# Kernel optimization log

Hardware: AMD Instinct MI355X
Metric: run time of the kernel (lower is better)

The kernel has to match this reference:

```python
import jax, jax.numpy as jnp
import numpy as np

B, H, W_SP, C = 256, 14, 14, 768
NUM_CLASSES = 701


def setup_inputs() -> dict:
    key = jax.random.key(0)
    k1, k2, k3 = jax.random.split(key, 3)
    x1 = jax.random.normal(k1, (B, H, W_SP, C), dtype=jnp.float32)
    x2 = jax.random.normal(k2, (B, H, W_SP, C), dtype=jnp.float32)
    W = jax.random.normal(k3, (C, NUM_CLASSES), dtype=jnp.float32) * 0.02
    b = jnp.zeros((NUM_CLASSES,), dtype=jnp.float32)
    return {"x1": x1, "x2": x2, "W": W, "b": b}


def _sgm(feats):
    """Vectorized SGM: per-sample sort by normalized token energy, gap-based
    split index, masked means for background/foreground. feats: [B, N, C]."""
    n = feats.shape[1]
    M = feats.sum(axis=-1)                                  # [B, N] token energies
    mn = M.min(axis=-1, keepdims=True)
    mx = M.max(axis=-1, keepdims=True)
    Mn = (M - mn) / (mx - mn)                               # normalized to [0,1]
    order = jnp.argsort(Mn, axis=-1)                        # ascending
    sorted_tens = jnp.take_along_axis(feats, order[:, :, None], axis=1)  # [B,N,C]
    sorted_M = jnp.take_along_axis(Mn, order, axis=-1)      # [B, N]
    # diff[j] = M[j+1]-M[j], forced to 0 where M[j]==0 (as in original)
    diff = jnp.where(sorted_M[:, :-1] == 0.0, 0.0,
                     sorted_M[:, 1:] - sorted_M[:, :-1])    # [B, N-1]
    k = jnp.argmax(diff, axis=-1)                           # [B] split index
    idx = jnp.arange(n)[None, :]                            # [1, N]
    fg_mask = (idx < k[:, None]).astype(feats.dtype)        # rows [:k] -> foreground
    bg_mask = 1.0 - fg_mask                                 # rows [k:] -> background
    fg_cnt = jnp.maximum(k.astype(feats.dtype), 1.0)[:, None]
    bg_cnt = jnp.maximum((n - k).astype(feats.dtype), 1.0)[:, None]
    foregr = jnp.einsum('bnc,bn->bc', sorted_tens, fg_mask) / fg_cnt
    backgr = jnp.einsum('bnc,bn->bc', sorted_tens, bg_mask) / bg_cnt
    return backgr, foregr


def reference(x1, x2, W, b):
    # flatten spatial dims into a token axis: [B, H*W, C]
    f1 = x1.reshape(x1.shape[0], -1, x1.shape[-1])
    f2 = x2.reshape(x2.shape[0], -1, x2.shape[-1])
    x1_bg, x1_fg = _sgm(f1)
    x2_bg, x2_fg = _sgm(f2)
    classif = lambda v: v @ W + b
    return (classif(x1_bg), classif(x1_fg), classif(x2_bg), classif(x2_fg))
```

## Files before the change

kernel.cpp:

```cpp
#include <hip/hip_runtime.h>
#include <hip/hip_bf16.h>

#define NTOK 196
#define CDIM 768
#define BSAMP 256
#define NCLS 701
#define NCLSP 704

typedef __attribute__((ext_vector_type(8))) short bf16x8;
typedef __attribute__((ext_vector_type(4))) float f32x4;

__device__ __forceinline__ void add4(float4& a, const float4& b) {
  a.x += b.x; a.y += b.y; a.z += b.z; a.w += b.w;
}

__global__ __launch_bounds__(512, 4) void sgm_kernel(const float* __restrict__ x1,
                                                     const float* __restrict__ x2,
                                                     __hip_bfloat16* __restrict__ Vb) {
  const int task = blockIdx.x;
  const int s  = task & 255;
  const int br = task >> 8;
  const float* __restrict__ feats = (br ? x2 : x1) + (size_t)s * (NTOK * CDIM);

  const int tid  = threadIdx.x;
  const int lane = tid & 63;
  const int wv   = tid >> 6;

  __shared__ __align__(16) float tokpart[NTOK][65];
  __shared__ float Msh[NTOK];
  __shared__ float Mn[NTOK];
  __shared__ float sortedv[NTOK];
  __shared__ int   rnk[NTOK];
  __shared__ int   list[NTOK];
  __shared__ float redmin[8], redmax[8];
  __shared__ int   kSh;
  __shared__ int   cntSh;
  float* partS = &tokpart[0][0];
  float* partT = partS + 8 * CDIM;

  float4 acc0 = {0,0,0,0}, acc1 = {0,0,0,0}, acc2 = {0,0,0,0};
  const float* lanebase = feats + lane * 4;

  int t = wv;
  for (; t + 8 < NTOK; t += 16) {
    const float* pA = lanebase + (size_t)t * CDIM;
    const float* pB = pA + (size_t)8 * CDIM;
    const float4 a0 = *(const float4*)(pA);
    const float4 a1 = *(const float4*)(pA + 256);
    const float4 a2 = *(const float4*)(pA + 512);
    const float4 b0 = *(const float4*)(pB);
    const float4 b1 = *(const float4*)(pB + 256);
    const float4 b2 = *(const float4*)(pB + 512);
    add4(acc0, a0); add4(acc1, a1); add4(acc2, a2);
    const float ea = ((a0.x + a0.y) + (a0.z + a0.w))
                   + ((a1.x + a1.y) + (a1.z + a1.w))
                   + ((a2.x + a2.y) + (a2.z + a2.w));
    tokpart[t][lane] = ea;
    add4(acc0, b0); add4(acc1, b1); add4(acc2, b2);
    const float eb = ((b0.x + b0.y) + (b0.z + b0.w))
                   + ((b1.x + b1.y) + (b1.z + b1.w))
                   + ((b2.x + b2.y) + (b2.z + b2.w));
    tokpart[t + 8][lane] = eb;
  }
  if (t < NTOK) {
    const float* pA = lanebase + (size_t)t * CDIM;
    const float4 a0 = *(const float4*)(pA);
    const float4 a1 = *(const float4*)(pA + 256);
    const float4 a2 = *(const float4*)(pA + 512);
    add4(acc0, a0); add4(acc1, a1); add4(acc2, a2);
    const float ea = ((a0.x + a0.y) + (a0.z + a0.w))
                   + ((a1.x + a1.y) + (a1.z + a1.w))
                   + ((a2.x + a2.y) + (a2.z + a2.w));
    tokpart[t][lane] = ea;
  }
  if (tid == 0) cntSh = 0;
  __syncthreads();

  for (int tt = wv; tt < NTOK; tt += 8) {
    float e = tokpart[tt][lane];
    #pragma unroll
    for (int off = 32; off; off >>= 1) e += __shfl_xor(e, off);
    if (lane == 0) Msh[tt] = e;
  }
  __syncthreads();

  float vmn = (tid < NTOK) ? Msh[tid] :  1e30f;
  float vmx = (tid < NTOK) ? Msh[tid] : -1e30f;
  #pragma unroll
  for (int off = 32; off; off >>= 1) {
    vmn = fminf(vmn, __shfl_xor(vmn, off));
    vmx = fmaxf(vmx, __shfl_xor(vmx, off));
  }
  if (lane == 0) { redmin[wv] = vmn; redmax[wv] = vmx; }
  __syncthreads();
  float mn = redmin[0], mx = redmax[0];
  #pragma unroll
  for (int i = 1; i < 8; i++) { mn = fminf(mn, redmin[i]); mx = fmaxf(mx, redmax[i]); }
  const float rng = mx - mn;
  if (tid < NTOK) Mn[tid] = (Msh[tid] - mn) / rng;
  __syncthreads();

  if (tid < NTOK) {
    const float mv = Mn[tid];
    int r = 0;
    for (int u = 0; u < NTOK; u++) {
      const float o = Mn[u];
      r += (o < mv) || (o == mv && u < tid);
    }
    sortedv[r] = mv;
    rnk[tid] = r;
  }
  __syncthreads();

  if (tid < 64) {
    float bd = -1.0f; int bj = NTOK;
    for (int j = lane; j < NTOK - 1; j += 64) {
      const float sj = sortedv[j];
      const float d = (sj == 0.0f) ? 0.0f : (sortedv[j + 1] - sj);
      if (d > bd || (d == bd && j < bj)) { bd = d; bj = j; }
    }
    #pragma unroll
    for (int off = 32; off; off >>= 1) {
      const float od = __shfl_xor(bd, off);
      const int   oj = __shfl_xor(bj, off);
      if (od > bd || (od == bd && oj < bj)) { bd = od; bj = oj; }
    }
    if (lane == 0) kSh = bj;
  }
  __syncthreads();

  const int k = kSh;
  const bool takeFg = (k <= NTOK / 2);

  if (tid < NTOK) {
    const int r = rnk[tid];
    const bool inSet = takeFg ? (r < k) : (r >= k);
    if (inSet) { int p = atomicAdd(&cntSh, 1); list[p] = tid; }
  }
  __syncthreads();
  const int m = cntSh;

  float4 t0a = {0,0,0,0}, t1a = {0,0,0,0}, t2a = {0,0,0,0};
  for (int i0 = wv * 4; i0 < m; i0 += 32) {
    const int nb = m - i0;
    float4 r[4][3];
    #pragma unroll
    for (int j = 0; j < 4; j++) {
      if (j < nb) {
        const int tk = list[i0 + j];
        const float* p = lanebase + (size_t)tk * CDIM;
        #pragma unroll
        for (int g = 0; g < 3; g++) r[j][g] = *(const float4*)(p + g * 256);
      }
    }
    #pragma unroll
    for (int j = 0; j < 4; j++) {
      if (j < nb) { add4(t0a, r[j][0]); add4(t1a, r[j][1]); add4(t2a, r[j][2]); }
    }
  }
  __syncthreads();

  const int base = lane * 4;
  *(float4*)&partS[wv * CDIM + base      ] = acc0;
  *(float4*)&partS[wv * CDIM + base + 256] = acc1;
  *(float4*)&partS[wv * CDIM + base + 512] = acc2;
  *(float4*)&partT[wv * CDIM + base      ] = t0a;
  *(float4*)&partT[wv * CDIM + base + 256] = t1a;
  *(float4*)&partT[wv * CDIM + base + 512] = t2a;
  __syncthreads();

  const float fgc = (float)(k > 1 ? k : 1);
  const float bgc = (float)((NTOK - k) > 1 ? (NTOK - k) : 1);
  const size_t rowFg = (size_t)(2 * br + 1) * BSAMP + s;
  const size_t rowBg = (size_t)(2 * br    ) * BSAMP + s;
  for (int c = tid; c < CDIM; c += 512) {
    float S = 0.0f, T = 0.0f;
    #pragma unroll
    for (int w = 0; w < 8; w++) { S += partS[w * CDIM + c]; T += partT[w * CDIM + c]; }
    float fg, bg;
    if (takeFg) { fg = T;     bg = S - T; }
    else        { bg = T;     fg = S - T; }
    Vb[rowFg * CDIM + c] = __float2bfloat16(fg / fgc);
    Vb[rowBg * CDIM + c] = __float2bfloat16(bg / bgc);
  }
}

__global__ __launch_bounds__(256) void wt_kernel(const float* __restrict__ W,
                                                 __hip_bfloat16* __restrict__ WT) {
  __shared__ float tile[32][33];
  const int c0 = blockIdx.x * 32;
  const int k0 = blockIdx.y * 32;
  const int tx = threadIdx.x & 31;
  const int ty = threadIdx.x >> 5;
  #pragma unroll
  for (int i = 0; i < 4; i++) {
    const int kr = ty + i * 8;
    const int c = c0 + tx;
    tile[kr][tx] = (c < NCLS) ? W[(size_t)(k0 + kr) * NCLS + c] : 0.0f;
  }
  __syncthreads();
  #pragma unroll
  for (int i = 0; i < 4; i++) {
    const int cr = ty + i * 8;
    const int cls = c0 + cr;
    WT[(size_t)cls * CDIM + k0 + tx] = __float2bfloat16(tile[tx][cr]);
  }
}

__global__ __launch_bounds__(256) void mfma_gemm(const __hip_bfloat16* __restrict__ Vb,
                                                 const __hip_bfloat16* __restrict__ WT,
                                                 const float* __restrict__ bias,
                                                 float* __restrict__ out) {
  const int w = blockIdx.x * 4 + (threadIdx.x >> 6);
  const int lane = threadIdx.x & 63;
  const int tr = w / (NCLSP / 16);
  const int tc = w % (NCLSP / 16);
  const int m0 = tr * 16;
  const int n0 = tc * 16;
  const int ko = (lane >> 4) * 8;

  const short* aptr = (const short*)Vb + (size_t)(m0 + (lane & 15)) * CDIM + ko;
  const short* bptr = (const short*)WT + (size_t)(n0 + (lane & 15)) * CDIM + ko;

  f32x4 acc = {0.f, 0.f, 0.f, 0.f};
  #pragma unroll
  for (int k0 = 0; k0 < CDIM; k0 += 32) {
    const bf16x8 af = *(const bf16x8*)(aptr + k0);
    const bf16x8 bf = *(const bf16x8*)(bptr + k0);
    acc = __builtin_amdgcn_mfma_f32_16x16x32_bf16(af, bf, acc, 0, 0, 0);
  }

  const int crow = m0 + (lane >> 4) * 4;
  const int ccol = n0 + (lane & 15);
  if (ccol < NCLS) {
    const float bv = bias[ccol];
    #pragma unroll
    for (int r = 0; r < 4; r++)
      out[(size_t)(crow + r) * NCLS + ccol] = acc[r] + bv;
  }
}

extern "C" void kernel_launch(void* const* d_in, const int* in_sizes, int n_in,
                              void* d_out, int out_size, void* d_ws, size_t ws_size,
                              hipStream_t stream) {
  const float* x1 = (const float*)d_in[0];
  const float* x2 = (const float*)d_in[1];
  const float* W  = (const float*)d_in[2];
  const float* b  = (const float*)d_in[3];
  float* out = (float*)d_out;

  __hip_bfloat16* Vb = (__hip_bfloat16*)d_ws;
  __hip_bfloat16* WT = (__hip_bfloat16*)((char*)d_ws + 1024 * CDIM * 2);

  sgm_kernel<<<512, 512, 0, stream>>>(x1, x2, Vb);
  wt_kernel<<<dim3(22, 24), 256, 0, stream>>>(W, WT);
  mfma_gemm<<<704, 256, 0, stream>>>(Vb, WT, b, out);
}
```

Measured before the change: 355.5 us.

## Split SGM into a quarter-token energy/colsum pass and a selection pass

The single SGM kernel becomes two kernels. The first uses 2048 blocks, each summing a quarter of a sample's tokens to produce token energies and partial column sums in global scratch. The second kernel reads those back, does the rank sort and split, and re-reads only the selected tokens from x. This spreads the main streaming read across four times as many blocks to raise memory-level parallelism, at the cost of an extra launch and some scratch traffic.

```diff
diff --git a/kernel.cpp b/kernel.cpp
--- a/kernel.cpp
+++ b/kernel.cpp
@@ -2,8 +2,10 @@
 #include <hip/hip_bf16.h>
 
 #define NTOK 196
+#define QTOK 49
 #define CDIM 768
 #define BSAMP 256
+#define NTASK 512
 #define NCLS 701
 #define NCLSP 704
 
@@ -14,9 +16,55 @@
   a.x += b.x; a.y += b.y; a.z += b.z; a.w += b.w;
 }
 
-__global__ __launch_bounds__(512, 4) void sgm_kernel(const float* __restrict__ x1,
-                                                     const float* __restrict__ x2,
-                                                     __hip_bfloat16* __restrict__ Vb) {
+__global__ __launch_bounds__(256, 8) void phaseA_kernel(const float* __restrict__ x1,
+                                                        const float* __restrict__ x2,
+                                                        float* __restrict__ Mg,
+                                                        float* __restrict__ Sg) {
+  const int b    = blockIdx.x;
+  const int task = b >> 2;
+  const int q    = b & 3;
+  const int s    = task & 255;
+  const int br   = task >> 8;
+  const float* __restrict__ feats = (br ? x2 : x1) + (size_t)s * (NTOK * CDIM);
+
+  const int tid  = threadIdx.x;
+  const int lane = tid & 63;
+  const int wv   = tid >> 6;
+
+  __shared__ float colred[4][CDIM];
+
+  float4 a0 = {0,0,0,0}, a1 = {0,0,0,0}, a2 = {0,0,0,0};
+  const float* lanebase = feats + (size_t)(q * QTOK) * CDIM + lane * 4;
+
+  for (int tl = wv; tl < QTOK; tl += 4) {
+    const float* p = lanebase + (size_t)tl * CDIM;
+    const float4 r0 = *(const float4*)(p);
+    const float4 r1 = *(const float4*)(p + 256);
+    const float4 r2 = *(const float4*)(p + 512);
+    add4(a0, r0); add4(a1, r1); add4(a2, r2);
+    float e = ((r0.x + r0.y) + (r0.z + r0.w))
+            + ((r1.x + r1.y) + (r1.z + r1.w))
+            + ((r2.x + r2.y) + (r2.z + r2.w));
+    #pragma unroll
+    for (int off = 32; off; off >>= 1) e += __shfl_xor(e, off);
+    if (lane == 0) Mg[(size_t)task * NTOK + q * QTOK + tl] = e;
+  }
+
+  *(float4*)&colred[wv][lane * 4      ] = a0;
+  *(float4*)&colred[wv][lane * 4 + 256] = a1;
+  *(float4*)&colred[wv][lane * 4 + 512] = a2;
+  __syncthreads();
+  for (int c = tid; c < CDIM; c += 256) {
+    Sg[(size_t)b * CDIM + c] = (colred[0][c] + colred[1][c])
+                             + (colred[2][c] + colred[3][c]);
+  }
+}
+
+__global__ __launch_bounds__(256) void sgm2_kernel(const float* __restrict__ x1,
+                                                   const float* __restrict__ x2,
+                                                   const float* __restrict__ Mg,
+                                                   const float* __restrict__ Sg,
+                                                   __hip_bfloat16* __restrict__ Vb) {
   const int task = blockIdx.x;
   const int s  = task & 255;
   const int br = task >> 8;
@@ -26,61 +74,25 @@
   const int lane = tid & 63;
   const int wv   = tid >> 6;
 
-  __shared__ __align__(16) float tokpart[NTOK][65];
   __shared__ float Msh[NTOK];
   __shared__ float Mn[NTOK];
   __shared__ float sortedv[NTOK];
   __shared__ int   rnk[NTOK];
   __shared__ int   list[NTOK];
-  __shared__ float redmin[8], redmax[8];
+  __shared__ float redmin[4], redmax[4];
   __shared__ int   kSh;
   __shared__ int   cntSh;
-  float* partS = &tokpart[0][0];
-  float* partT = partS + 8 * CDIM;
-
-  float4 acc0 = {0,0,0,0}, acc1 = {0,0,0,0}, acc2 = {0,0,0,0};
-  const float* lanebase = feats + lane * 4;
-
-  int t = wv;
-  for (; t + 8 < NTOK; t += 16) {
-    const float* pA = lanebase + (size_t)t * CDIM;
-    const float* pB = pA + (size_t)8 * CDIM;
-    const float4 a0 = *(const float4*)(pA);
-    const float4 a1 = *(const float4*)(pA + 256);
-    const float4 a2 = *(const float4*)(pA + 512);
-    const float4 b0 = *(const float4*)(pB);
-    const float4 b1 = *(const float4*)(pB + 256);
-    const float4 b2 = *(const float4*)(pB + 512);
-    add4(acc0, a0); add4(acc1, a1); add4(acc2, a2);
-    const float ea = ((a0.x + a0.y) + (a0.z + a0.w))
-                   + ((a1.x + a1.y) + (a1.z + a1.w))
-                   + ((a2.x + a2.y) + (a2.z + a2.w));
-    tokpart[t][lane] = ea;
-    add4(acc0, b0); add4(acc1, b1); add4(acc2, b2);
-    const float eb = ((b0.x + b0.y) + (b0.z + b0.w))
-                   + ((b1.x + b1.y) + (b1.z + b1.w))
-                   + ((b2.x + b2.y) + (b2.z + b2.w));
-    tokpart[t + 8][lane] = eb;
-  }
-  if (t < NTOK) {
-    const float* pA = lanebase + (size_t)t * CDIM;
-    const float4 a0 = *(const float4*)(pA);
-    const float4 a1 = *(const float4*)(pA + 256);
-    const float4 a2 = *(const float4*)(pA + 512);
-    add4(acc0, a0); add4(acc1, a1); add4(acc2, a2);
-    const float ea = ((a0.x + a0.y) + (a0.z + a0.w))
-                   + ((a1.x + a1.y) + (a1.z + a1.w))
-                   + ((a2.x + a2.y) + (a2.z + a2.w));
-    tokpart[t][lane] = ea;
-  }
+  __shared__ float partT[4][CDIM];
+
+  if (tid < NTOK) Msh[tid] = Mg[(size_t)task * NTOK + tid];
   if (tid == 0) cntSh = 0;
-  __syncthreads();
-
-  for (int tt = wv; tt < NTOK; tt += 8) {
-    float e = tokpart[tt][lane];
-    #pragma unroll
-    for (int off = 32; off; off >>= 1) e += __shfl_xor(e, off);
-    if (lane == 0) Msh[tt] = e;
+
+  float srow[3];
+  #pragma unroll
+  for (int j = 0; j < 3; j++) {
+    const int c = tid + j * 256;
+    const float* sq = Sg + (size_t)(task * 4) * CDIM + c;
+    srow[j] = (sq[0] + sq[CDIM]) + (sq[2 * CDIM] + sq[3 * CDIM]);
   }
   __syncthreads();
 
@@ -95,7 +107,7 @@
   __syncthreads();
   float mn = redmin[0], mx = redmax[0];
   #pragma unroll
-  for (int i = 1; i < 8; i++) { mn = fminf(mn, redmin[i]); mx = fmaxf(mx, redmax[i]); }
+  for (int i = 1; i < 4; i++) { mn = fminf(mn, redmin[i]); mx = fmaxf(mx, redmax[i]); }
   const float rng = mx - mn;
   if (tid < NTOK) Mn[tid] = (Msh[tid] - mn) / rng;
   __syncthreads();
@@ -141,7 +153,8 @@
   const int m = cntSh;
 
   float4 t0a = {0,0,0,0}, t1a = {0,0,0,0}, t2a = {0,0,0,0};
-  for (int i0 = wv * 4; i0 < m; i0 += 32) {
+  const float* lanebase = feats + lane * 4;
+  for (int i0 = wv * 4; i0 < m; i0 += 16) {
     const int nb = m - i0;
     float4 r[4][3];
     #pragma unroll
@@ -158,25 +171,21 @@
       if (j < nb) { add4(t0a, r[j][0]); add4(t1a, r[j][1]); add4(t2a, r[j][2]); }
     }
   }
-  __syncthreads();
-
-  const int base = lane * 4;
-  *(float4*)&partS[wv * CDIM + base      ] = acc0;
-  *(float4*)&partS[wv * CDIM + base + 256] = acc1;
-  *(float4*)&partS[wv * CDIM + base + 512] = acc2;
-  *(float4*)&partT[wv * CDIM + base      ] = t0a;
-  *(float4*)&partT[wv * CDIM + base + 256] = t1a;
-  *(float4*)&partT[wv * CDIM + base + 512] = t2a;
+
+  *(float4*)&partT[wv][lane * 4      ] = t0a;
+  *(float4*)&partT[wv][lane * 4 + 256] = t1a;
+  *(float4*)&partT[wv][lane * 4 + 512] = t2a;
   __syncthreads();
 
   const float fgc = (float)(k > 1 ? k : 1);
   const float bgc = (float)((NTOK - k) > 1 ? (NTOK - k) : 1);
   const size_t rowFg = (size_t)(2 * br + 1) * BSAMP + s;
   const size_t rowBg = (size_t)(2 * br    ) * BSAMP + s;
-  for (int c = tid; c < CDIM; c += 512) {
-    float S = 0.0f, T = 0.0f;
-    #pragma unroll
-    for (int w = 0; w < 8; w++) { S += partS[w * CDIM + c]; T += partT[w * CDIM + c]; }
+  #pragma unroll
+  for (int j = 0; j < 3; j++) {
+    const int c = tid + j * 256;
+    const float T = (partT[0][c] + partT[1][c]) + (partT[2][c] + partT[3][c]);
+    const float S = srow[j];
     float fg, bg;
     if (takeFg) { fg = T;     bg = S - T; }
     else        { bg = T;     fg = S - T; }
@@ -249,10 +258,14 @@
   const float* b  = (const float*)d_in[3];
   float* out = (float*)d_out;
 
-  __hip_bfloat16* Vb = (__hip_bfloat16*)d_ws;
-  __hip_bfloat16* WT = (__hip_bfloat16*)((char*)d_ws + 1024 * CDIM * 2);
-
-  sgm_kernel<<<512, 512, 0, stream>>>(x1, x2, Vb);
+  char* ws = (char*)d_ws;
+  __hip_bfloat16* Vb = (__hip_bfloat16*)ws;
+  __hip_bfloat16* WT = (__hip_bfloat16*)(ws + 1572864);
+  float* Mg = (float*)(ws + 1572864 + 1081344);
+  float* Sg = (float*)(ws + 1572864 + 1081344 + 401408);
+
+  phaseA_kernel<<<2048, 256, 0, stream>>>(x1, x2, Mg, Sg);
+  sgm2_kernel<<<512, 256, 0, stream>>>(x1, x2, Mg, Sg, Vb);
   wt_kernel<<<dim3(22, 24), 256, 0, stream>>>(W, WT);
   mfma_gemm<<<704, 256, 0, stream>>>(Vb, WT, b, out);
 }
```

Result: no change. 353.3 us (-0.6%).
